# Performance work log

Hardware: AMD Instinct MI355X
Metric: run time of the kernel (lower is better)

Reference implementation:

```python
import jax, jax.numpy as jnp
import numpy as np

B, V, NX, R, D, H = 512, 2, 1024, 64, 512, 8
S, NC, HS = 4, 2, 64           # bc_state_dim, num_controls, state-branch hidden
FIN = S * HS + 128             # fusion input dim (state feats + control feats)


def _ln(x, g, b, eps=1e-5):
    mu = jnp.mean(x, axis=-1, keepdims=True)
    var = jnp.mean((x - mu) ** 2, axis=-1, keepdims=True)
    return (x - mu) * jax.lax.rsqrt(var + eps) * g + b


def setup_inputs() -> dict:
    key = jax.random.key(0)
    ks = iter(jax.random.split(key, 64))
    def rn(shape, s=0.02):
        return jax.random.normal(next(ks), shape, dtype=jnp.float32) * s
    inp = {}
    inp['a_n'] = jax.random.normal(next(ks), (B, V, R), dtype=jnp.float32)
    inp['BC_Ctrl'] = jax.random.normal(next(ks), (B, S + NC), dtype=jnp.float32)
    inp['Phi'] = rn((V, NX, R), 1.0 / np.sqrt(NX).astype(np.float32))
    # per-variable attention params (stacked on leading V axis)
    inp['Wq_w'] = rn((V, 1, D));   inp['Wq_b'] = rn((V, D))
    inp['Wk_w'] = rn((V, NX, D));  inp['Wk_b'] = rn((V, D))
    inp['Wv_w'] = rn((V, NX, D));  inp['Wv_b'] = rn((V, D))
    inp['attn_ow'] = rn((V, D, D)); inp['attn_ob'] = rn((V, D))
    inp['proj_w'] = rn((V, D, 1));  inp['proj_b'] = rn((V, 1))
    # ImprovedUpdateFFN (num_layers=3, hidden=d_model) + LayerNorm
    inp['ffn_w1'] = rn((V, R, D)); inp['ffn_b1'] = rn((V, D))
    inp['ffn_w2'] = rn((V, D, D)); inp['ffn_b2'] = rn((V, D))
    inp['ffn_w3'] = rn((V, D, R)); inp['ffn_b3'] = rn((V, R))
    inp['ffn_ln_g'] = jnp.ones((V, R), jnp.float32)
    inp['ffn_ln_b'] = jnp.zeros((V, R), jnp.float32)
    # a0_mapping: Linear -> ReLU -> LayerNorm
    inp['a0_w'] = rn((V, R, R)); inp['a0_b'] = rn((V, R))
    inp['a0_ln_g'] = jnp.ones((V, R), jnp.float32)
    inp['a0_ln_b'] = jnp.zeros((V, R), jnp.float32)
    inp['alpha'] = jnp.full((V,), 0.1, jnp.float32)
    # UniversalLifting params
    inp['sb_w'] = rn((S, 1, HS)); inp['sb_b'] = rn((S, HS))
    inp['cm_w1'] = rn((NC, 64));  inp['cm_b1'] = rn((64,))
    inp['cm_w2'] = rn((64, 128)); inp['cm_b2'] = rn((128,))
    inp['fu_w1'] = rn((FIN, 256)); inp['fu_b1'] = rn((256,))
    inp['fu_w2'] = rn((256, 512)); inp['fu_b2'] = rn((512,))
    inp['fu_w3'] = rn((512, 256)); inp['fu_b3'] = rn((256,))
    inp['fu_w4'] = rn((256, V * NX)); inp['fu_b4'] = rn((V * NX,))
    return inp


def reference(a_n, BC_Ctrl, Phi, Wq_w, Wq_b, Wk_w, Wk_b, Wv_w, Wv_b,
              attn_ow, attn_ob, proj_w, proj_b,
              ffn_w1, ffn_b1, ffn_w2, ffn_b2, ffn_w3, ffn_b3, ffn_ln_g, ffn_ln_b,
              a0_w, a0_b, a0_ln_g, a0_ln_b, alpha,
              sb_w, sb_b, cm_w1, cm_b1, cm_w2, cm_b2,
              fu_w1, fu_b1, fu_w2, fu_b2, fu_w3, fu_b3, fu_w4, fu_b4):
    gelu = jax.nn.gelu
    # ---- UniversalLifting: U_B [B, V, NX] ----
    bs = BC_Ctrl[:, :S]                                              # [B,S]
    sf = gelu(bs[:, :, None] * sb_w[None, :, 0, :] + sb_b[None])     # [B,S,HS]
    sf = sf.reshape(bs.shape[0], S * HS)
    cf = gelu(BC_Ctrl[:, S:] @ cm_w1 + cm_b1)
    cf = gelu(cf @ cm_w2 + cm_b2)
    f = jnp.concatenate([sf, cf], axis=-1)                           # [B,FIN]
    h = gelu(f @ fu_w1 + fu_b1)
    h = gelu(h @ fu_w2 + fu_b2)
    h = gelu(h @ fu_w3 + fu_b3)
    U_B = (h @ fu_w4 + fu_b4).reshape(-1, V, NX)
    # ---- a0 mapping: Linear -> ReLU -> LayerNorm ----
    a_map = jax.nn.relu(jnp.einsum('bvr,vrs->bvs', a_n, a0_w) + a0_b[None])
    a_map = _ln(a_map, a0_ln_g[None], a0_ln_b[None])                 # [B,V,R]
    # ---- ImprovedUpdateFFN residual update ----
    h1 = gelu(jnp.einsum('bvr,vrd->bvd', a_map, ffn_w1) + ffn_b1[None])
    h2 = gelu(jnp.einsum('bvd,vde->bve', h1, ffn_w2) + ffn_b2[None])
    o = jnp.einsum('bvd,vdr->bvr', h2, ffn_w3) + ffn_b3[None]
    ffn_update = _ln(o + a_map, ffn_ln_g[None], ffn_ln_b[None])      # [B,V,R]
    # ---- Q/K/V; K,V depend only on Phi (batch-independent) ----
    Q = a_map[:, :, :, None] * Wq_w[:, 0][None, :, None, :] + Wq_b[None, :, None, :]  # [B,V,R,D]
    K = jnp.einsum('vnr,vnd->vrd', Phi, Wk_w) + Wk_b[:, None, :]     # [V,R,D]
    Vm = jnp.einsum('vnr,vnd->vrd', Phi, Wv_w) + Wv_b[:, None, :]    # [V,R,D]
    hd = D // H
    Qh = Q.reshape(-1, V, R, H, hd)
    Kh = K.reshape(V, R, H, hd)
    Vh = Vm.reshape(V, R, H, hd)
    # softmax-free linear attention: z = Q (K^T V) per head
    KV = jnp.einsum('vrhk,vrhl->vhkl', Kh, Vh)                        # [V,H,hd,hd]
    z = jnp.einsum('bvrhk,vhkl->bvrhl', Qh, KV).reshape(-1, V, R, D)
    z = jnp.einsum('bvrd,vde->bvre', z, attn_ow) + attn_ob[None, :, None, :]
    z = z / jnp.sqrt(jnp.float32(D))
    a_update = jnp.einsum('bvrd,vdo->bvro', z, proj_w)[..., 0] + proj_b[:, 0][None, :, None]
    a_next = a_map + a_update + alpha[None, :, None] * ffn_update     # [B,V,R]
    U_hat = jnp.einsum('vnr,bvr->bvn', Phi, a_next) + U_B             # [B,V,NX]
    return U_hat
```

## Files before the change

### kernel.cpp

```cpp
#include <hip/hip_runtime.h>
#include <hip/hip_bf16.h>
#include <math.h>


typedef unsigned short ushort_t;
using short8 = __attribute__((ext_vector_type(8))) short;
using f32x4  = __attribute__((ext_vector_type(4))) float;

__device__ __forceinline__ float gelu_f(float x) {
    float x3 = x*x*x;
    return 0.5f*x*(1.0f + tanhf(0.7978845608028654f*(x + 0.044715f*x3)));
}

__device__ __forceinline__ float wave_sum(float x) {
    #pragma unroll
    for (int m = 32; m >= 1; m >>= 1) x += __shfl_xor(x, m, 64);
    return x;
}

__device__ __forceinline__ ushort_t f2bf(float x) {
    unsigned u = __float_as_uint(x);
    unsigned r = (u + 0x7FFFu + ((u >> 16) & 1u)) >> 16;
    return (ushort_t)r;
}
__device__ __forceinline__ float bf2f(ushort_t h) {
    return __uint_as_float(((unsigned)h) << 16);
}

struct Ptrs {
    const float *a_n, *BC, *Phi, *Wq_w, *Wq_b, *Wk_w, *Wk_b, *Wv_w, *Wv_b,
                *attn_ow, *attn_ob, *proj_w, *proj_b,
                *ffn_w3, *ffn_b3, *ffn_ln_g, *ffn_ln_b,
                *a0_w, *a0_b, *a0_ln_g, *a0_ln_b, *alpha,
                *sb_w, *sb_b, *cm_w1, *cm_b1, *cm_w2, *cm_b2,
                *fu_b1, *fu_b2, *fu_b3, *fu_b4, *ffn_b1, *ffn_b2;
    float *opj, *u0, *u1, *u2, *pkq, *pqq, *pvo, *phirs, *bias2, *out;
    ushort_t *amap_bf, *h1_bf, *h2_bf, *fbuf_bf, *hA_bf, *hB_bf;
    ushort_t *w_fu1t, *w_fu2t, *w_fu3t, *w_ffn1t, *w_ffn2t, *Abig, *Bbig;
};

struct CvtDesc { const float* src; ushort_t* dst; int K, N, mode, ldd, coff; };
struct CvtArgs { CvtDesc d[10]; int cum[11]; };

__device__ void cvt_dev(char* smem, int tile, const CvtDesc& d, const Ptrs& p)
{
    const int t = threadIdx.x;
    if (d.mode == 2) {
        const int row = t >> 2, q = t & 3;
        const float* s = d.src + (long)(tile*64 + row)*64 + q*16;
        ushort_t* dst  = d.dst + (long)(tile*64 + row)*384 + d.coff + q*16;
        ushort_t* dz   = d.dst + (long)(tile*64 + row)*384 + (64 - d.coff) + q*16;
        float sum = 0.f;
        #pragma unroll
        for (int i = 0; i < 4; ++i) {
            float4 x = *(const float4*)(s + i*4);
            ushort4 w; w.x=f2bf(x.x); w.y=f2bf(x.y); w.z=f2bf(x.z); w.w=f2bf(x.w);
            *(ushort4*)(dst + i*4) = w;
            ushort4 z; z.x=0; z.y=0; z.z=0; z.w=0;
            *(ushort4*)(dz + i*4) = z;
            sum += x.x + x.y + x.z + x.w;
        }
        sum += __shfl_xor(sum, 1, 64);
        sum += __shfl_xor(sum, 2, 64);
        if (q == 0) p.phirs[d.K + tile*64 + row] = sum;
    } else {
        float* tl = (float*)smem;
        const int ntn = d.N >> 5;
        const int kt = tile / ntn, nt = tile % ntn;
        const int r = t >> 3, c0 = (t & 7) * 4;
        float4 v = *(const float4*)(d.src + (long)(kt*32 + r)*d.N + nt*32 + c0);
        tl[r*33 + c0] = v.x; tl[r*33 + c0+1] = v.y;
        tl[r*33 + c0+2] = v.z; tl[r*33 + c0+3] = v.w;
        __syncthreads();
        ushort4 w;
        w.x = f2bf(tl[(c0+0)*33 + r]); w.y = f2bf(tl[(c0+1)*33 + r]);
        w.z = f2bf(tl[(c0+2)*33 + r]); w.w = f2bf(tl[(c0+3)*33 + r]);
        *(ushort4*)(d.dst + (long)(nt*32 + r)*d.ldd + d.coff + kt*32 + c0) = w;
    }
}

__device__ void bgemm_dev(char* smem_,
    const ushort_t* __restrict__ A, const ushort_t* __restrict__ B,
    const float* __restrict__ bias,
    void* __restrict__ Cv, int m0, int n0, int K, int ldc,
    int EPI, bool OUTBF)
{
    ushort_t* lds = (ushort_t*)smem_;
    const int tid = threadIdx.x;
    const int w = tid >> 6, l = tid & 63;
    const int ml = l & 15, kg = l >> 4;
    const int srow = tid >> 2, sslot = tid & 3;
    const ushort_t* Ag = A + (long)(m0 + srow)*K + sslot*8;
    const ushort_t* Bg = B + (long)(n0 + srow)*K + sslot*8;
    auto L = [&](int buf, int ab, int row, int col) {
        return lds + (((buf*2 + ab)*64 + row)*40 + col);
    };
    f32x4 acc[4] = {};
    const int nt = K >> 5;
    int4 ra = *(const int4*)Ag;
    int4 rb = *(const int4*)Bg;
    *(int4*)L(0,0,srow,sslot*8) = ra;
    *(int4*)L(0,1,srow,sslot*8) = rb;
    __syncthreads();
    for (int t = 0; t < nt; ++t) {
        const int cur = t & 1;
        if (t + 1 < nt) {
            ra = *(const int4*)(Ag + (t+1)*32);
            rb = *(const int4*)(Bg + (t+1)*32);
        }
        short8 af = *(const short8*)L(cur,0,w*16 + ml,kg*8);
        #pragma unroll
        for (int f = 0; f < 4; ++f) {
            short8 bfr = *(const short8*)L(cur,1,f*16 + ml,kg*8);
            acc[f] = __builtin_amdgcn_mfma_f32_16x16x32_bf16(af, bfr, acc[f], 0, 0, 0);
        }
        if (t + 1 < nt) {
            *(int4*)L(cur^1,0,srow,sslot*8) = ra;
            *(int4*)L(cur^1,1,srow,sslot*8) = rb;
            __syncthreads();
        }
    }
    float* Cf = (float*)Cv; ushort_t* Cb = (ushort_t*)Cv;
    const int mr = m0 + w*16 + kg*4;
    const int nc = n0 + ml;
    #pragma unroll
    for (int f = 0; f < 4; ++f) {
        const int n = nc + f*16;
        const float bs = bias[n];
        #pragma unroll
        for (int r = 0; r < 4; ++r) {
            float x = acc[f][r] + bs;
            if (EPI == 1) x = gelu_f(x);
            if (OUTBF) Cb[(long)(mr + r)*ldc + n] = f2bf(x);
            else       Cf[(long)(mr + r)*ldc + n] = x;
        }
    }
}

__device__ void control_dev(char* smem, int b, const Ptrs& p)
{
    float* bc  = (float*)smem;
    float* cf1 = bc + 8;
    const int tid = threadIdx.x;
    if (tid < 6) bc[tid] = p.BC[b*6 + tid];
    __syncthreads();
    {
        int s = tid >> 6;
        p.fbuf_bf[(long)b*384 + tid] = f2bf(gelu_f(bc[s]*p.sb_w[tid] + p.sb_b[tid]));
    }
    if (tid < 64) {
        cf1[tid] = gelu_f(bc[4]*p.cm_w1[tid] + bc[5]*p.cm_w1[64+tid] + p.cm_b1[tid]);
    }
    __syncthreads();
    if (tid < 128) {
        float acc = p.cm_b2[tid];
        #pragma unroll 8
        for (int i = 0; i < 64; ++i) acc = fmaf(cf1[i], p.cm_w2[i*128 + tid], acc);
        p.fbuf_bf[(long)b*384 + 256 + tid] = f2bf(gelu_f(acc));
    }
}

__device__ void a_map_dev(char* smem, int bx, int v, const Ptrs& p)
{
    float* arow = (float*)smem;
    const int w = threadIdx.x >> 6, lane = threadIdx.x & 63;
    const int b = bx*4 + w;
    arow[w*64 + lane] = p.a_n[((long)b*2 + v)*64 + lane];
    __syncthreads();
    float acc = p.a0_b[v*64 + lane];
    #pragma unroll 8
    for (int rp = 0; rp < 64; ++rp)
        acc = fmaf(arow[w*64 + rp], p.a0_w[((long)v*64 + rp)*64 + lane], acc);
    float x = fmaxf(acc, 0.0f);
    float mu = wave_sum(x) * (1.0f/64.0f);
    float d = x - mu;
    float var = wave_sum(d*d) * (1.0f/64.0f);
    float y = d * rsqrtf(var + 1e-5f) * p.a0_ln_g[v*64 + lane] + p.a0_ln_b[v*64 + lane];
    p.amap_bf[((long)v*512 + b)*64 + lane] = f2bf(y);
}

__device__ void opj_dev(int oi, const Ptrs& p)
{
    const int tid = threadIdx.x;
    const int v = oi >> 3, dc = oi & 7;
    const int d = dc*64 + (tid >> 2);
    const int e0 = (tid & 3)*128;
    const float* row = p.attn_ow + ((long)v*512 + d)*512 + e0;
    const float* pj  = p.proj_w + v*512 + e0;
    float s = 0.f;
    #pragma unroll 8
    for (int j = 0; j < 128; ++j) s = fmaf(row[j], pj[j], s);
    s += __shfl_xor(s, 1, 64);
    s += __shfl_xor(s, 2, 64);
    if ((tid & 3) == 0) p.opj[v*512 + d] = s;
}

__device__ void u01_dev(int i, const Ptrs& p)
{
    const int tid = threadIdx.x;
    const int w = tid >> 6, lane = tid & 63;
    const int v = i >> 4, c = i & 15;
    const float* wq = p.Wq_w + v*512;
    const float* wb = p.Wq_b + v*512;
    for (int pass = 0; pass < 16; ++pass) {
        const int n = c*64 + pass*4 + w;
        const float* row = p.Wk_w + ((long)v*1024 + n)*512 + lane*8;
        float4 a = *(const float4*)row, b = *(const float4*)(row + 4);
        float s0 = 0.f, s1 = 0.f;
        #pragma unroll
        for (int j = 0; j < 8; ++j) {
            float x = (j < 4) ? ((const float*)&a)[j] : ((const float*)&b)[j-4];
            s0 = fmaf(x, wq[lane*8 + j], s0);
            s1 = fmaf(x, wb[lane*8 + j], s1);
        }
        s0 += __shfl_xor(s0,1,64); s0 += __shfl_xor(s0,2,64); s0 += __shfl_xor(s0,4,64);
        s1 += __shfl_xor(s1,1,64); s1 += __shfl_xor(s1,2,64); s1 += __shfl_xor(s1,4,64);
        if ((lane & 7) == 0) {
            const int h = lane >> 3;
            p.u0[((long)v*1024 + n)*8 + h] = s0;
            p.u1[((long)v*1024 + n)*8 + h] = s1;
        }
    }
}

__device__ void u2_dev(int i, const Ptrs& p)
{
    const int tid = threadIdx.x;
    const int w = tid >> 6, lane = tid & 63;
    const int v = i >> 4, c = i & 15;
    const float* oj = p.opj + v*512;
    for (int pass = 0; pass < 16; ++pass) {
        const int n = c*64 + pass*4 + w;
        const float* row = p.Wv_w + ((long)v*1024 + n)*512 + lane*8;
        float4 a = *(const float4*)row, b = *(const float4*)(row + 4);
        float s0 = 0.f;
        #pragma unroll
        for (int j = 0; j < 8; ++j) {
            float x = (j < 4) ? ((const float*)&a)[j] : ((const float*)&b)[j-4];
            s0 = fmaf(x, oj[lane*8 + j], s0);
        }
        s0 += __shfl_xor(s0,1,64); s0 += __shfl_xor(s0,2,64); s0 += __shfl_xor(s0,4,64);
        if ((lane & 7) == 0) p.u2[((long)v*1024 + n)*8 + (lane >> 3)] = s0;
    }
}

__device__ void kqqq_dev(int i, const Ptrs& p)
{
    const int tid = threadIdx.x;
    const int v = i >> 3, c = i & 7;
    const int r = tid & 63, hp = tid >> 6;
    const int h0 = hp*2, h1 = h0 + 1;
    float k0=0.f,k1=0.f,q0=0.f,q1=0.f;
    const float* Pb = p.Phi + ((long)v*1024 + c*128)*64 + r;
    const float* U0 = p.u0 + ((long)v*1024 + c*128)*8;
    const float* U1 = p.u1 + ((long)v*1024 + c*128)*8;
    #pragma unroll 4
    for (int n = 0; n < 128; ++n) {
        float phi = Pb[(long)n*64];
        k0 = fmaf(phi, U0[n*8+h0], k0); k1 = fmaf(phi, U0[n*8+h1], k1);
        q0 = fmaf(phi, U1[n*8+h0], q0); q1 = fmaf(phi, U1[n*8+h1], q1);
    }
    const long o = (((long)v*8 + c)*64 + r)*8;
    p.pkq[o+h0] = k0; p.pkq[o+h1] = k1;
    p.pqq[o+h0] = q0; p.pqq[o+h1] = q1;
}

__device__ void pvo_dev(int i, const Ptrs& p)
{
    const int tid = threadIdx.x;
    const int v = i >> 3, c = i & 7;
    const int r = tid & 63, hp = tid >> 6;
    const int h0 = hp*2, h1 = h0 + 1;
    float a0 = 0.f, a1 = 0.f;
    const float* Pb = p.Phi + ((long)v*1024 + c*128)*64 + r;
    const float* U2 = p.u2 + ((long)v*1024 + c*128)*8;
    #pragma unroll 4
    for (int n = 0; n < 128; ++n) {
        float phi = Pb[(long)n*64];
        a0 = fmaf(phi, U2[n*8+h0], a0);
        a1 = fmaf(phi, U2[n*8+h1], a1);
    }
    const long o = (((long)v*8 + c)*64 + r)*8;
    p.pvo[o+h0] = a0; p.pvo[o+h1] = a1;
}

__device__ float2 consts_final_dev(char* smem, int v, const Ptrs& p)
{
    const int tid = threadIdx.x;
    const int r = tid & 63, hp = tid >> 6;
    const int h0 = hp*2, h1 = h0 + 1;
    float k0=0.f,k1=0.f,q0=0.f,q1=0.f,w0=0.f,w1=0.f;
    #pragma unroll
    for (int c = 0; c < 8; ++c) {
        const long o = (((long)v*8 + c)*64 + r)*8;
        k0 += p.pkq[o+h0]; k1 += p.pkq[o+h1];
        q0 += p.pqq[o+h0]; q1 += p.pqq[o+h1];
        w0 += p.pvo[o+h0]; w1 += p.pvo[o+h1];
    }
    float bk0=0.f,bk1=0.f,bq0=0.f,bq1=0.f,bv0=0.f,bv1=0.f;
    #pragma unroll 8
    for (int j = 0; j < 64; ++j) {
        float b0 = p.Wk_b[v*512 + h0*64 + j], b1 = p.Wk_b[v*512 + h1*64 + j];
        bk0 = fmaf(b0, p.Wq_w[v*512 + h0*64 + j], bk0);
        bk1 = fmaf(b1, p.Wq_w[v*512 + h1*64 + j], bk1);
        bq0 = fmaf(b0, p.Wq_b[v*512 + h0*64 + j], bq0);
        bq1 = fmaf(b1, p.Wq_b[v*512 + h1*64 + j], bq1);
        float c0v = p.Wv_b[v*512 + h0*64 + j], c1v = p.Wv_b[v*512 + h1*64 + j];
        bv0 = fmaf(c0v, p.opj[v*512 + h0*64 + j], bv0);
        bv1 = fmaf(c1v, p.opj[v*512 + h1*64 + j], bv1);
    }
    w0 += bv0; w1 += bv1;
    k0 += bk0; k1 += bk1; q0 += bq0; q1 += bq1;
    float s1 = k0*w0 + k1*w1;
    float s0 = q0*w0 + q1*w1;
    float sA = p.attn_ob[v*512 + tid]*p.proj_w[v*512 + tid]
             + p.attn_ob[v*512 + 256 + tid]*p.proj_w[v*512 + 256 + tid];
    s1 = wave_sum(s1); s0 = wave_sum(s0); sA = wave_sum(sA);
    float* red = (float*)smem;
    const int w = tid >> 6, l = tid & 63;
    __syncthreads();
    if (l == 0) { red[w] = s1; red[4+w] = s0; red[8+w] = sA; }
    __syncthreads();
    float S1 = red[0]+red[1]+red[2]+red[3];
    float S0 = red[4]+red[5]+red[6]+red[7];
    float SA = red[8]+red[9]+red[10]+red[11];
    __syncthreads();
    const float inv = 0.044194173824159216f;
    float2 res;
    res.x = S1*inv;
    res.y = (S0 + SA)*inv + p.proj_b[v];
    return res;
}

__device__ void ofuse_dev(char* smem, int bx, int v, const Ptrs& p)
{
    const float c1 = consts_final_dev(smem, v, p).x;
    float* hrow = (float*)smem;
    const int w = threadIdx.x >> 6, lane = threadIdx.x & 63;
    const int b = bx*4 + w;
    const ushort_t* h2p = p.h2_bf + ((long)v*512 + b)*512;
    #pragma unroll
    for (int i = 0; i < 8; ++i) hrow[w*512 + lane + i*64] = bf2f(h2p[lane + i*64]);
    __syncthreads();
    float acc = p.ffn_b3[v*64 + lane];
    const float* w3p = p.ffn_w3 + (long)v*512*64 + lane;
    #pragma unroll 8
    for (int d = 0; d < 512; ++d)
        acc = fmaf(hrow[w*512 + d], w3p[(long)d*64], acc);
    const float am = bf2f(p.amap_bf[((long)v*512 + b)*64 + lane]);
    float t = acc + am;
    float mu = wave_sum(t) * (1.0f/64.0f);
    float dd = t - mu;
    float var = wave_sum(dd*dd) * (1.0f/64.0f);
    float u = dd * rsqrtf(var + 1e-5f) * p.ffn_ln_g[v*64+lane] + p.ffn_ln_b[v*64+lane];
    p.Abig[(long)b*384 + v*64 + lane] = f2bf(am*(1.0f + c1) + p.alpha[v]*u);
}

__device__ void bias2_dev(char* smem, const Ptrs& p)
{
    const float c00 = consts_final_dev(smem, 0, p).y;
    const float c01 = consts_final_dev(smem, 1, p).y;
    #pragma unroll
    for (int k = 0; k < 8; ++k) {
        const int n2 = k*256 + threadIdx.x;
        const float c0 = (n2 >> 10) ? c01 : c00;
        p.bias2[n2] = p.fu_b4[n2] + c0*p.phirs[n2];
    }
}

__global__ __launch_bounds__(256) void stage0_k(Ptrs p, CvtArgs ca, int ncvt)
{
    extern __shared__ char smem[];
    const int bx = blockIdx.x;
    if (bx < ncvt) {
        int e = 0;
        while (bx >= ca.cum[e+1]) ++e;
        cvt_dev(smem, bx - ca.cum[e], ca.d[e], p);
    } else if (bx < ncvt + 512) {
        control_dev(smem, bx - ncvt, p);
    } else if (bx < ncvt + 768) {
        int i = bx - ncvt - 512;
        a_map_dev(smem, i & 127, i >> 7, p);
    } else if (bx < ncvt + 784) {
        opj_dev(bx - ncvt - 768, p);
    } else {
        u01_dev(bx - ncvt - 784, p);
    }
}

__global__ __launch_bounds__(256) void stage1_k(Ptrs p)
{
    extern __shared__ char smem[];
    const int bx = blockIdx.x;
    if (bx < 32) {
        bgemm_dev(smem, p.fbuf_bf, p.w_fu1t, p.fu_b1, p.hA_bf,
                  (bx>>2)*64, (bx&3)*64, 384, 256, 1, true);
    } else if (bx < 160) {
        int i = bx - 32; int v = i >> 6; i &= 63;
        bgemm_dev(smem, p.amap_bf + (long)v*32768, p.w_ffn1t + (long)v*32768,
                  p.ffn_b1 + v*512, (void*)(p.h1_bf + (long)v*262144),
                  (i>>3)*64, (i&7)*64, 64, 512, 1, true);
    } else if (bx < 192) {
        u2_dev(bx - 160, p);
    } else {
        kqqq_dev(bx - 192, p);
    }
}

__global__ __launch_bounds__(256) void stage2_k(Ptrs p)
{
    extern __shared__ char smem[];
    const int bx = blockIdx.x;
    if (bx < 64) {
        bgemm_dev(smem, p.hA_bf, p.w_fu2t, p.fu_b2, p.hB_bf,
                  (bx>>3)*64, (bx&7)*64, 256, 512, 1, true);
    } else if (bx < 192) {
        int i = bx - 64; int v = i >> 6; i &= 63;
        bgemm_dev(smem, p.h1_bf + (long)v*262144, p.w_ffn2t + (long)v*262144,
                  p.ffn_b2 + v*512, (void*)(p.h2_bf + (long)v*262144),
                  (i>>3)*64, (i&7)*64, 512, 512, 1, true);
    } else {
        pvo_dev(bx - 192, p);
    }
}

__global__ __launch_bounds__(256) void stage3_k(Ptrs p)
{
    extern __shared__ char smem[];
    const int bx = blockIdx.x;
    if (bx < 32) {
        bgemm_dev(smem, p.hB_bf, p.w_fu3t, p.fu_b3, (void*)(p.Abig + 128),
                  (bx>>2)*64, (bx&3)*64, 512, 384, 1, true);
    } else if (bx < 288) {
        int i = bx - 32;
        ofuse_dev(smem, i & 127, i >> 7, p);
    } else {
        bias2_dev(smem, p);
    }
}

__global__ __launch_bounds__(256) void stage4_k(Ptrs p)
{
    extern __shared__ char smem[];
    const int bx = blockIdx.x;
    bgemm_dev(smem, p.Abig, p.Bbig, p.bias2, (void*)p.out,
              (bx>>5)*64, (bx&31)*64, 384, 2048, 0, false);
}

extern "C" void kernel_launch(void* const* d_in, const int* in_sizes, int n_in,
                              void* d_out, int out_size, void* d_ws, size_t ws_size,
                              hipStream_t stream)
{
    const float* a_n      = (const float*)d_in[0];
    const float* BC       = (const float*)d_in[1];
    const float* Phi      = (const float*)d_in[2];
    const float* Wq_w     = (const float*)d_in[3];
    const float* Wq_b     = (const float*)d_in[4];
    const float* Wk_w     = (const float*)d_in[5];
    const float* Wk_b     = (const float*)d_in[6];
    const float* Wv_w     = (const float*)d_in[7];
    const float* Wv_b     = (const float*)d_in[8];
    const float* attn_ow  = (const float*)d_in[9];
    const float* attn_ob  = (const float*)d_in[10];
    const float* proj_w   = (const float*)d_in[11];
    const float* proj_b   = (const float*)d_in[12];
    const float* ffn_w1   = (const float*)d_in[13];
    const float* ffn_b1   = (const float*)d_in[14];
    const float* ffn_w2   = (const float*)d_in[15];
    const float* ffn_b2   = (const float*)d_in[16];
    const float* ffn_w3   = (const float*)d_in[17];
    const float* ffn_b3   = (const float*)d_in[18];
    const float* ffn_ln_g = (const float*)d_in[19];
    const float* ffn_ln_b = (const float*)d_in[20];
    const float* a0_w     = (const float*)d_in[21];
    const float* a0_b     = (const float*)d_in[22];
    const float* a0_ln_g  = (const float*)d_in[23];
    const float* a0_ln_b  = (const float*)d_in[24];
    const float* alpha    = (const float*)d_in[25];
    const float* sb_w     = (const float*)d_in[26];
    const float* sb_b     = (const float*)d_in[27];
    const float* cm_w1    = (const float*)d_in[28];
    const float* cm_b1    = (const float*)d_in[29];
    const float* cm_w2    = (const float*)d_in[30];
    const float* cm_b2    = (const float*)d_in[31];
    const float* fu_w1    = (const float*)d_in[32];
    const float* fu_b1    = (const float*)d_in[33];
    const float* fu_w2    = (const float*)d_in[34];
    const float* fu_b2    = (const float*)d_in[35];
    const float* fu_w3    = (const float*)d_in[36];
    const float* fu_b3    = (const float*)d_in[37];
    const float* fu_w4    = (const float*)d_in[38];
    const float* fu_b4    = (const float*)d_in[39];

    float* ws = (float*)d_ws;
    Ptrs p;
    p.a_n = a_n; p.BC = BC; p.Phi = Phi; p.Wq_w = Wq_w; p.Wq_b = Wq_b;
    p.Wk_w = Wk_w; p.Wk_b = Wk_b; p.Wv_w = Wv_w; p.Wv_b = Wv_b;
    p.attn_ow = attn_ow; p.attn_ob = attn_ob; p.proj_w = proj_w; p.proj_b = proj_b;
    p.ffn_w3 = ffn_w3; p.ffn_b3 = ffn_b3; p.ffn_ln_g = ffn_ln_g; p.ffn_ln_b = ffn_ln_b;
    p.a0_w = a0_w; p.a0_b = a0_b; p.a0_ln_g = a0_ln_g; p.a0_ln_b = a0_ln_b;
    p.alpha = alpha; p.sb_w = sb_w; p.sb_b = sb_b;
    p.cm_w1 = cm_w1; p.cm_b1 = cm_b1; p.cm_w2 = cm_w2; p.cm_b2 = cm_b2;
    p.fu_b1 = fu_b1; p.fu_b2 = fu_b2; p.fu_b3 = fu_b3; p.fu_b4 = fu_b4;
    p.ffn_b1 = ffn_b1; p.ffn_b2 = ffn_b2;

    p.opj     = ws;
    p.u0      = ws + 1024;
    p.u1      = ws + 17408;
    p.u2      = ws + 33792;
    p.pkq     = ws + 50176;
    p.pqq     = ws + 58368;
    p.pvo     = ws + 66560;
    p.phirs   = ws + 74752;
    p.bias2   = ws + 76800;
    p.amap_bf = (ushort_t*)(ws + 78848);
    p.h1_bf   = (ushort_t*)(ws + 111616);
    p.h2_bf   = (ushort_t*)(ws + 373760);
    p.fbuf_bf = (ushort_t*)(ws + 635904);
    p.hA_bf   = (ushort_t*)(ws + 734208);
    p.hB_bf   = (ushort_t*)(ws + 799744);
    p.w_fu1t  = (ushort_t*)(ws + 930816);
    p.w_fu2t  = (ushort_t*)(ws + 979968);
    p.w_fu3t  = (ushort_t*)(ws + 1045504);
    p.w_ffn1t = (ushort_t*)(ws + 1111040);
    p.w_ffn2t = (ushort_t*)(ws + 1143808);
    p.Abig    = (ushort_t*)(ws + 1405952);
    p.Bbig    = (ushort_t*)(ws + 1504256);
    p.out     = (float*)d_out;

    CvtArgs ca;
    auto set = [&](int i, const float* s, ushort_t* dst, int K, int N,
                   int mode, int ldd, int coff) {
        ca.d[i].src = s; ca.d[i].dst = dst; ca.d[i].K = K; ca.d[i].N = N;
        ca.d[i].mode = mode; ca.d[i].ldd = ldd; ca.d[i].coff = coff;
    };
    set(0, fu_w1,            p.w_fu1t,           384, 256,  0, 384, 0);
    set(1, fu_w2,            p.w_fu2t,           256, 512,  0, 256, 0);
    set(2, fu_w3,            p.w_fu3t,           512, 256,  0, 512, 0);
    set(3, fu_w4,            p.Bbig,             256, 2048, 0, 384, 128);
    set(4, ffn_w1,           p.w_ffn1t,          64,  512,  0, 64,  0);
    set(5, ffn_w1 + 32768,   p.w_ffn1t + 32768,  64,  512,  0, 64,  0);
    set(6, ffn_w2,           p.w_ffn2t,          512, 512,  0, 512, 0);
    set(7, ffn_w2 + 262144,  p.w_ffn2t + 262144, 512, 512,  0, 512, 0);
    set(8, Phi,              p.Bbig,             0,    0,   2, 384, 0);
    set(9, Phi + 65536,      p.Bbig + (long)1024*384, 1024, 0, 2, 384, 64);
    const int tl[10] = {96,128,128,512,32,32,256,256,16,16};
    ca.cum[0] = 0;
    for (int i = 0; i < 10; ++i) ca.cum[i+1] = ca.cum[i] + tl[i];
    const int ncvt = ca.cum[10];

    stage0_k<<<ncvt + 816, 256, 4352,  stream>>>(p, ca, ncvt);
    stage1_k<<<208,        256, 20480, stream>>>(p);
    stage2_k<<<208,        256, 20480, stream>>>(p);
    stage3_k<<<289,        256, 20480, stream>>>(p);
    stage4_k<<<256,        256, 20480, stream>>>(p);
}
```

Baseline: 78.55 us.

## Replace scalar FFN output layer with bf16 MFMA GEMM plus separate LayerNorm pass

The FFN third layer (h2 @ ffn_w3) used to run as a per-row scalar FMA loop with fused LayerNorm. It now runs as a bf16 tiled GEMM in stage3 on pre-converted transposed weights. A new small kernel then applies residual, LayerNorm and the alpha blend, reading the attention constants that bias2_dev saves to a workspace slot. This moves the work onto matrix cores, at the cost of an extra launch, an fp32 intermediate round trip, extra weight conversion in stage0, and bf16 rounding of ffn_w3.

```diff
diff --git a/kernel.cpp b/kernel.cpp
--- a/kernel.cpp
+++ b/kernel.cpp
@@ -34,13 +34,15 @@
                 *a0_w, *a0_b, *a0_ln_g, *a0_ln_b, *alpha,
                 *sb_w, *sb_b, *cm_w1, *cm_b1, *cm_w2, *cm_b2,
                 *fu_b1, *fu_b2, *fu_b3, *fu_b4, *ffn_b1, *ffn_b2;
-    float *opj, *u0, *u1, *u2, *pkq, *pqq, *pvo, *phirs, *bias2, *out;
+    float *opj, *u0, *u1, *u2, *pkq, *pqq, *pvo, *phirs, *bias2, *parts,
+          *obuf, *out;
     ushort_t *amap_bf, *h1_bf, *h2_bf, *fbuf_bf, *hA_bf, *hB_bf;
-    ushort_t *w_fu1t, *w_fu2t, *w_fu3t, *w_ffn1t, *w_ffn2t, *Abig, *Bbig;
+    ushort_t *w_fu1t, *w_fu2t, *w_fu3t, *w_ffn1t, *w_ffn2t, *w_ffn3t,
+             *Abig, *Bbig;
 };
 
 struct CvtDesc { const float* src; ushort_t* dst; int K, N, mode, ldd, coff; };
-struct CvtArgs { CvtDesc d[10]; int cum[11]; };
+struct CvtArgs { CvtDesc d[12]; int cum[13]; };
 
 __device__ void cvt_dev(char* smem, int tile, const CvtDesc& d, const Ptrs& p)
 {
@@ -332,38 +334,18 @@
     return res;
 }
 
-__device__ void ofuse_dev(char* smem, int bx, int v, const Ptrs& p)
-{
-    const float c1 = consts_final_dev(smem, v, p).x;
-    float* hrow = (float*)smem;
-    const int w = threadIdx.x >> 6, lane = threadIdx.x & 63;
-    const int b = bx*4 + w;
-    const ushort_t* h2p = p.h2_bf + ((long)v*512 + b)*512;
-    #pragma unroll
-    for (int i = 0; i < 8; ++i) hrow[w*512 + lane + i*64] = bf2f(h2p[lane + i*64]);
-    __syncthreads();
-    float acc = p.ffn_b3[v*64 + lane];
-    const float* w3p = p.ffn_w3 + (long)v*512*64 + lane;
-    #pragma unroll 8
-    for (int d = 0; d < 512; ++d)
-        acc = fmaf(hrow[w*512 + d], w3p[(long)d*64], acc);
-    const float am = bf2f(p.amap_bf[((long)v*512 + b)*64 + lane]);
-    float t = acc + am;
-    float mu = wave_sum(t) * (1.0f/64.0f);
-    float dd = t - mu;
-    float var = wave_sum(dd*dd) * (1.0f/64.0f);
-    float u = dd * rsqrtf(var + 1e-5f) * p.ffn_ln_g[v*64+lane] + p.ffn_ln_b[v*64+lane];
-    p.Abig[(long)b*384 + v*64 + lane] = f2bf(am*(1.0f + c1) + p.alpha[v]*u);
-}
-
 __device__ void bias2_dev(char* smem, const Ptrs& p)
 {
-    const float c00 = consts_final_dev(smem, 0, p).y;
-    const float c01 = consts_final_dev(smem, 1, p).y;
+    const float2 cv0 = consts_final_dev(smem, 0, p);
+    const float2 cv1 = consts_final_dev(smem, 1, p);
+    if (threadIdx.x == 0) {
+        p.parts[0] = cv0.x; p.parts[1] = cv1.x;
+        p.parts[2] = cv0.y; p.parts[3] = cv1.y;
+    }
     #pragma unroll
     for (int k = 0; k < 8; ++k) {
         const int n2 = k*256 + threadIdx.x;
-        const float c0 = (n2 >> 10) ? c01 : c00;
+        const float c0 = (n2 >> 10) ? cv1.y : cv0.y;
         p.bias2[n2] = p.fu_b4[n2] + c0*p.phirs[n2];
     }
 }
@@ -431,12 +413,30 @@
     if (bx < 32) {
         bgemm_dev(smem, p.hB_bf, p.w_fu3t, p.fu_b3, (void*)(p.Abig + 128),
                   (bx>>2)*64, (bx&3)*64, 512, 384, 1, true);
-    } else if (bx < 288) {
-        int i = bx - 32;
-        ofuse_dev(smem, i & 127, i >> 7, p);
+    } else if (bx < 48) {
+        int i = bx - 32; int v = i >> 3; int m = i & 7;
+        bgemm_dev(smem, p.h2_bf + (long)v*262144, p.w_ffn3t + (long)v*32768,
+                  p.ffn_b3 + v*64, (void*)(p.obuf + (long)v*32768),
+                  m*64, 0, 512, 64, 0, false);
     } else {
         bias2_dev(smem, p);
     }
+}
+
+__global__ __launch_bounds__(256) void stage3b_k(Ptrs p)
+{
+    const int g = blockIdx.x*4 + (threadIdx.x >> 6);
+    const int lane = threadIdx.x & 63;
+    const int v = g >> 9, b = g & 511;
+    const float o  = p.obuf[((long)v*512 + b)*64 + lane];
+    const float am = bf2f(p.amap_bf[((long)v*512 + b)*64 + lane]);
+    float t = o + am;
+    float mu = wave_sum(t) * (1.0f/64.0f);
+    float dd = t - mu;
+    float var = wave_sum(dd*dd) * (1.0f/64.0f);
+    float u = dd * rsqrtf(var + 1e-5f) * p.ffn_ln_g[v*64+lane] + p.ffn_ln_b[v*64+lane];
+    const float c1 = p.parts[v];
+    p.Abig[(long)b*384 + v*64 + lane] = f2bf(am*(1.0f + c1) + p.alpha[v]*u);
 }
 
 __global__ __launch_bounds__(256) void stage4_k(Ptrs p)
@@ -513,19 +513,22 @@
     p.pvo     = ws + 66560;
     p.phirs   = ws + 74752;
     p.bias2   = ws + 76800;
-    p.amap_bf = (ushort_t*)(ws + 78848);
-    p.h1_bf   = (ushort_t*)(ws + 111616);
-    p.h2_bf   = (ushort_t*)(ws + 373760);
-    p.fbuf_bf = (ushort_t*)(ws + 635904);
-    p.hA_bf   = (ushort_t*)(ws + 734208);
-    p.hB_bf   = (ushort_t*)(ws + 799744);
-    p.w_fu1t  = (ushort_t*)(ws + 930816);
-    p.w_fu2t  = (ushort_t*)(ws + 979968);
-    p.w_fu3t  = (ushort_t*)(ws + 1045504);
-    p.w_ffn1t = (ushort_t*)(ws + 1111040);
-    p.w_ffn2t = (ushort_t*)(ws + 1143808);
-    p.Abig    = (ushort_t*)(ws + 1405952);
-    p.Bbig    = (ushort_t*)(ws + 1504256);
+    p.parts   = ws + 78848;
+    p.amap_bf = (ushort_t*)(ws + 78976);
+    p.h1_bf   = (ushort_t*)(ws + 111744);
+    p.h2_bf   = (ushort_t*)(ws + 373888);
+    p.fbuf_bf = (ushort_t*)(ws + 636032);
+    p.hA_bf   = (ushort_t*)(ws + 734336);
+    p.hB_bf   = (ushort_t*)(ws + 799872);
+    p.w_fu1t  = (ushort_t*)(ws + 930944);
+    p.w_fu2t  = (ushort_t*)(ws + 980096);
+    p.w_fu3t  = (ushort_t*)(ws + 1045632);
+    p.w_ffn1t = (ushort_t*)(ws + 1111168);
+    p.w_ffn2t = (ushort_t*)(ws + 1143936);
+    p.w_ffn3t = (ushort_t*)(ws + 1406080);
+    p.Abig    = (ushort_t*)(ws + 1438848);
+    p.Bbig    = (ushort_t*)(ws + 1537152);
+    p.obuf    = ws + 1930368;
     p.out     = (float*)d_out;
 
     CvtArgs ca;
@@ -534,24 +537,27 @@
         ca.d[i].src = s; ca.d[i].dst = dst; ca.d[i].K = K; ca.d[i].N = N;
         ca.d[i].mode = mode; ca.d[i].ldd = ldd; ca.d[i].coff = coff;
     };
-    set(0, fu_w1,            p.w_fu1t,           384, 256,  0, 384, 0);
-    set(1, fu_w2,            p.w_fu2t,           256, 512,  0, 256, 0);
-    set(2, fu_w3,            p.w_fu3t,           512, 256,  0, 512, 0);
-    set(3, fu_w4,            p.Bbig,             256, 2048, 0, 384, 128);
-    set(4, ffn_w1,           p.w_ffn1t,          64,  512,  0, 64,  0);
-    set(5, ffn_w1 + 32768,   p.w_ffn1t + 32768,  64,  512,  0, 64,  0);
-    set(6, ffn_w2,           p.w_ffn2t,          512, 512,  0, 512, 0);
-    set(7, ffn_w2 + 262144,  p.w_ffn2t + 262144, 512, 512,  0, 512, 0);
-    set(8, Phi,              p.Bbig,             0,    0,   2, 384, 0);
-    set(9, Phi + 65536,      p.Bbig + (long)1024*384, 1024, 0, 2, 384, 64);
-    const int tl[10] = {96,128,128,512,32,32,256,256,16,16};
+    set(0,  fu_w1,           p.w_fu1t,           384, 256,  0, 384, 0);
+    set(1,  fu_w2,           p.w_fu2t,           256, 512,  0, 256, 0);
+    set(2,  fu_w3,           p.w_fu3t,           512, 256,  0, 512, 0);
+    set(3,  fu_w4,           p.Bbig,             256, 2048, 0, 384, 128);
+    set(4,  ffn_w1,          p.w_ffn1t,          64,  512,  0, 64,  0);
+    set(5,  ffn_w1 + 32768,  p.w_ffn1t + 32768,  64,  512,  0, 64,  0);
+    set(6,  ffn_w2,          p.w_ffn2t,          512, 512,  0, 512, 0);
+    set(7,  ffn_w2 + 262144, p.w_ffn2t + 262144, 512, 512,  0, 512, 0);
+    set(8,  Phi,             p.Bbig,             0,    0,   2, 384, 0);
+    set(9,  Phi + 65536,     p.Bbig + (long)1024*384, 1024, 0, 2, 384, 64);
+    set(10, ffn_w3,          p.w_ffn3t,          512, 64,   0, 512, 0);
+    set(11, ffn_w3 + 32768,  p.w_ffn3t + 32768,  512, 64,   0, 512, 0);
+    const int tl[12] = {96,128,128,512,32,32,256,256,16,16,32,32};
     ca.cum[0] = 0;
-    for (int i = 0; i < 10; ++i) ca.cum[i+1] = ca.cum[i] + tl[i];
-    const int ncvt = ca.cum[10];
-
-    stage0_k<<<ncvt + 816, 256, 4352,  stream>>>(p, ca, ncvt);
-    stage1_k<<<208,        256, 20480, stream>>>(p);
-    stage2_k<<<208,        256, 20480, stream>>>(p);
-    stage3_k<<<289,        256, 20480, stream>>>(p);
-    stage4_k<<<256,        256, 20480, stream>>>(p);
-}
+    for (int i = 0; i < 12; ++i) ca.cum[i+1] = ca.cum[i] + tl[i];
+    const int ncvt = ca.cum[12];
+
+    stage0_k <<<ncvt + 816, 256, 4352,  stream>>>(p, ca, ncvt);
+    stage1_k <<<208,        256, 20480, stream>>>(p);
+    stage2_k <<<208,        256, 20480, stream>>>(p);
+    stage3_k <<<49,         256, 20480, stream>>>(p);
+    stage3b_k<<<256,        256, 0,     stream>>>(p);
+    stage4_k <<<256,        256, 20480, stream>>>(p);
+}
```

Result: faster. 71.10 us (-9.5%).

## Replace scalar FFN output layer with bf16 MFMA GEMM fused with LayerNorm

Applied to the files above, without the earlier changes.

The per-row scalar FMA loop for the FFN third layer (h2 @ ffn_w3) is replaced by a tiled bf16 MFMA GEMM, 64-row tiles with double-buffered LDS. Bias, residual add, LayerNorm and the alpha blend are applied in the epilogue. ffn_w3 is now converted to transposed bf16 in stage0, which adds conversion tiles and shifts workspace offsets. Stage3 launches far fewer blocks (49 vs 289), so fewer CUs are busy, and the layer now runs at bf16 rather than fp32 precision.

```diff
diff --git a/kernel.cpp b/kernel.cpp
--- a/kernel.cpp
+++ b/kernel.cpp
@@ -36,11 +36,12 @@
                 *fu_b1, *fu_b2, *fu_b3, *fu_b4, *ffn_b1, *ffn_b2;
     float *opj, *u0, *u1, *u2, *pkq, *pqq, *pvo, *phirs, *bias2, *out;
     ushort_t *amap_bf, *h1_bf, *h2_bf, *fbuf_bf, *hA_bf, *hB_bf;
-    ushort_t *w_fu1t, *w_fu2t, *w_fu3t, *w_ffn1t, *w_ffn2t, *Abig, *Bbig;
+    ushort_t *w_fu1t, *w_fu2t, *w_fu3t, *w_ffn1t, *w_ffn2t, *w_ffn3t,
+             *Abig, *Bbig;
 };
 
 struct CvtDesc { const float* src; ushort_t* dst; int K, N, mode, ldd, coff; };
-struct CvtArgs { CvtDesc d[10]; int cum[11]; };
+struct CvtArgs { CvtDesc d[12]; int cum[13]; };
 
 __device__ void cvt_dev(char* smem, int tile, const CvtDesc& d, const Ptrs& p)
 {
@@ -332,28 +333,75 @@
     return res;
 }
 
-__device__ void ofuse_dev(char* smem, int bx, int v, const Ptrs& p)
-{
-    const float c1 = consts_final_dev(smem, v, p).x;
-    float* hrow = (float*)smem;
-    const int w = threadIdx.x >> 6, lane = threadIdx.x & 63;
-    const int b = bx*4 + w;
-    const ushort_t* h2p = p.h2_bf + ((long)v*512 + b)*512;
-    #pragma unroll
-    for (int i = 0; i < 8; ++i) hrow[w*512 + lane + i*64] = bf2f(h2p[lane + i*64]);
-    __syncthreads();
-    float acc = p.ffn_b3[v*64 + lane];
-    const float* w3p = p.ffn_w3 + (long)v*512*64 + lane;
-    #pragma unroll 8
-    for (int d = 0; d < 512; ++d)
-        acc = fmaf(hrow[w*512 + d], w3p[(long)d*64], acc);
-    const float am = bf2f(p.amap_bf[((long)v*512 + b)*64 + lane]);
-    float t = acc + am;
-    float mu = wave_sum(t) * (1.0f/64.0f);
-    float dd = t - mu;
-    float var = wave_sum(dd*dd) * (1.0f/64.0f);
-    float u = dd * rsqrtf(var + 1e-5f) * p.ffn_ln_g[v*64+lane] + p.ffn_ln_b[v*64+lane];
-    p.Abig[(long)b*384 + v*64 + lane] = f2bf(am*(1.0f + c1) + p.alpha[v]*u);
+__device__ void ogemm_ln_dev(char* smem_, int v, int m0, const Ptrs& p)
+{
+    const float c1 = consts_final_dev(smem_, v, p).x;
+
+    ushort_t* lds = (ushort_t*)smem_;
+    const int tid = threadIdx.x;
+    const int w = tid >> 6, l = tid & 63;
+    const int ml = l & 15, kg = l >> 4;
+    const int srow = tid >> 2, sslot = tid & 3;
+    const ushort_t* A = p.h2_bf + (long)v*262144;
+    const ushort_t* B = p.w_ffn3t + (long)v*32768;
+    const float* bias = p.ffn_b3 + v*64;
+    const ushort_t* Ag = A + (long)(m0 + srow)*512 + sslot*8;
+    const ushort_t* Bg = B + (long)srow*512 + sslot*8;
+    auto L = [&](int buf, int ab, int row, int col) {
+        return lds + (((buf*2 + ab)*64 + row)*40 + col);
+    };
+    f32x4 acc[4] = {};
+    int4 ra = *(const int4*)Ag;
+    int4 rb = *(const int4*)Bg;
+    *(int4*)L(0,0,srow,sslot*8) = ra;
+    *(int4*)L(0,1,srow,sslot*8) = rb;
+    __syncthreads();
+    for (int t = 0; t < 16; ++t) {
+        const int cur = t & 1;
+        if (t + 1 < 16) {
+            ra = *(const int4*)(Ag + (t+1)*32);
+            rb = *(const int4*)(Bg + (t+1)*32);
+        }
+        short8 af = *(const short8*)L(cur,0,w*16 + ml,kg*8);
+        #pragma unroll
+        for (int f = 0; f < 4; ++f) {
+            short8 bfr = *(const short8*)L(cur,1,f*16 + ml,kg*8);
+            acc[f] = __builtin_amdgcn_mfma_f32_16x16x32_bf16(af, bfr, acc[f], 0, 0, 0);
+        }
+        if (t + 1 < 16) {
+            *(int4*)L(cur^1,0,srow,sslot*8) = ra;
+            *(int4*)L(cur^1,1,srow,sslot*8) = rb;
+            __syncthreads();
+        }
+    }
+    __syncthreads();
+    float* ot = (float*)smem_;
+    {
+        const int rl = w*16 + kg*4;
+        #pragma unroll
+        for (int f = 0; f < 4; ++f) {
+            const int n = ml + f*16;
+            const float bs = bias[n];
+            #pragma unroll
+            for (int r = 0; r < 4; ++r)
+                ot[(rl + r)*66 + n] = acc[f][r] + bs;
+        }
+    }
+    __syncthreads();
+    const float g  = p.ffn_ln_g[v*64 + l];
+    const float bt = p.ffn_ln_b[v*64 + l];
+    const float al = p.alpha[v];
+    for (int rr = 0; rr < 16; ++rr) {
+        const int row = w*16 + rr;
+        const int b = m0 + row;
+        const float am = bf2f(p.amap_bf[((long)v*512 + b)*64 + l]);
+        float t = ot[row*66 + l] + am;
+        float mu = wave_sum(t) * (1.0f/64.0f);
+        float dd = t - mu;
+        float var = wave_sum(dd*dd) * (1.0f/64.0f);
+        float u = dd * rsqrtf(var + 1e-5f) * g + bt;
+        p.Abig[(long)b*384 + v*64 + l] = f2bf(am*(1.0f + c1) + al*u);
+    }
 }
 
 __device__ void bias2_dev(char* smem, const Ptrs& p)
@@ -431,9 +479,9 @@
     if (bx < 32) {
         bgemm_dev(smem, p.hB_bf, p.w_fu3t, p.fu_b3, (void*)(p.Abig + 128),
                   (bx>>2)*64, (bx&3)*64, 512, 384, 1, true);
-    } else if (bx < 288) {
+    } else if (bx < 48) {
         int i = bx - 32;
-        ofuse_dev(smem, i & 127, i >> 7, p);
+        ogemm_ln_dev(smem, i >> 3, (i & 7)*64, p);
     } else {
         bias2_dev(smem, p);
     }
@@ -524,8 +572,9 @@
     p.w_fu3t  = (ushort_t*)(ws + 1045504);
     p.w_ffn1t = (ushort_t*)(ws + 1111040);
     p.w_ffn2t = (ushort_t*)(ws + 1143808);
-    p.Abig    = (ushort_t*)(ws + 1405952);
-    p.Bbig    = (ushort_t*)(ws + 1504256);
+    p.w_ffn3t = (ushort_t*)(ws + 1405952);
+    p.Abig    = (ushort_t*)(ws + 1438720);
+    p.Bbig    = (ushort_t*)(ws + 1537024);
     p.out     = (float*)d_out;
 
     CvtArgs ca;
@@ -534,24 +583,26 @@
         ca.d[i].src = s; ca.d[i].dst = dst; ca.d[i].K = K; ca.d[i].N = N;
         ca.d[i].mode = mode; ca.d[i].ldd = ldd; ca.d[i].coff = coff;
     };
-    set(0, fu_w1,            p.w_fu1t,           384, 256,  0, 384, 0);
-    set(1, fu_w2,            p.w_fu2t,           256, 512,  0, 256, 0);
-    set(2, fu_w3,            p.w_fu3t,           512, 256,  0, 512, 0);
-    set(3, fu_w4,            p.Bbig,             256, 2048, 0, 384, 128);
-    set(4, ffn_w1,           p.w_ffn1t,          64,  512,  0, 64,  0);
-    set(5, ffn_w1 + 32768,   p.w_ffn1t + 32768,  64,  512,  0, 64,  0);
-    set(6, ffn_w2,           p.w_ffn2t,          512, 512,  0, 512, 0);
-    set(7, ffn_w2 + 262144,  p.w_ffn2t + 262144, 512, 512,  0, 512, 0);
-    set(8, Phi,              p.Bbig,             0,    0,   2, 384, 0);
-    set(9, Phi + 65536,      p.Bbig + (long)1024*384, 1024, 0, 2, 384, 64);
-    const int tl[10] = {96,128,128,512,32,32,256,256,16,16};
+    set(0,  fu_w1,           p.w_fu1t,           384, 256,  0, 384, 0);
+    set(1,  fu_w2,           p.w_fu2t,           256, 512,  0, 256, 0);
+    set(2,  fu_w3,           p.w_fu3t,           512, 256,  0, 512, 0);
+    set(3,  fu_w4,           p.Bbig,             256, 2048, 0, 384, 128);
+    set(4,  ffn_w1,          p.w_ffn1t,          64,  512,  0, 64,  0);
+    set(5,  ffn_w1 + 32768,  p.w_ffn1t + 32768,  64,  512,  0, 64,  0);
+    set(6,  ffn_w2,          p.w_ffn2t,          512, 512,  0, 512, 0);
+    set(7,  ffn_w2 + 262144, p.w_ffn2t + 262144, 512, 512,  0, 512, 0);
+    set(8,  Phi,             p.Bbig,             0,    0,   2, 384, 0);
+    set(9,  Phi + 65536,     p.Bbig + (long)1024*384, 1024, 0, 2, 384, 64);
+    set(10, ffn_w3,          p.w_ffn3t,          512, 64,   0, 512, 0);
+    set(11, ffn_w3 + 32768,  p.w_ffn3t + 32768,  512, 64,   0, 512, 0);
+    const int tl[12] = {96,128,128,512,32,32,256,256,16,16,32,32};
     ca.cum[0] = 0;
-    for (int i = 0; i < 10; ++i) ca.cum[i+1] = ca.cum[i] + tl[i];
-    const int ncvt = ca.cum[10];
+    for (int i = 0; i < 12; ++i) ca.cum[i+1] = ca.cum[i] + tl[i];
+    const int ncvt = ca.cum[12];
 
     stage0_k<<<ncvt + 816, 256, 4352,  stream>>>(p, ca, ncvt);
     stage1_k<<<208,        256, 20480, stream>>>(p);
     stage2_k<<<208,        256, 20480, stream>>>(p);
-    stage3_k<<<289,        256, 20480, stream>>>(p);
+    stage3_k<<<49,         256, 20480, stream>>>(p);
     stage4_k<<<256,        256, 20480, stream>>>(p);
 }
```

After: 75.06 us. 4.4% less time.
